# Kernel tuning notes

Measured on AMD Instinct MI355X. Metric: run time of the kernel, lower is better.

The kernel has to match this reference:

```python
import jax, jax.numpy as jnp
import numpy as np

CONF_THRES = 0.5   # self.conf_thres
NMS_THRES = 0.5    # self.nms_thres
PRE_NMS = 2048     # candidates kept before pairwise IoU
MAX_DET = 300      # padded detections returned per image
MAX_WH = 4096.0    # class-offset trick so NMS is per-class
IMG_SIZE = 416.0   # self.img_size; boxes_scale (416,416)->(416,416) => scale 1


def xywh2xyxy(b):
    xy, wh = b[..., :2], b[..., 2:4]
    return jnp.concatenate([xy - wh * 0.5, xy + wh * 0.5], axis=-1)


def pairwise_iou(boxes):
    # boxes: [K,4] xyxy -> [K,K] IoU
    area = (boxes[:, 2] - boxes[:, 0]) * (boxes[:, 3] - boxes[:, 1])
    lt = jnp.maximum(boxes[:, None, :2], boxes[None, :, :2])
    rb = jnp.minimum(boxes[:, None, 2:], boxes[None, :, 2:])
    wh = jnp.clip(rb - lt, 0.0)
    inter = wh[..., 0] * wh[..., 1]
    return inter / (area[:, None] + area[None, :] - inter + 1e-16)


def nms_single(pred):
    # pred: [N,85] = xywh(4) + objectness(1) + class scores(80)
    boxes = xywh2xyxy(pred[:, :4])
    obj = pred[:, 4]
    cls_scores = pred[:, 5:] * obj[:, None]        # conf = obj * class prob
    conf = jnp.max(cls_scores, axis=-1)
    cls_id = jnp.argmax(cls_scores, axis=-1)
    valid = obj >= CONF_THRES                      # confidence threshold filter
    score = jnp.where(valid, conf, -1.0)

    order = jnp.argsort(-score)[:PRE_NMS]          # sort desc, keep top PRE_NMS
    boxes_s = boxes[order]
    score_s = score[order]
    cls_s = cls_id[order]
    valid_s = valid[order]

    # per-class NMS via coordinate offset by class id
    off = cls_s.astype(boxes_s.dtype) * MAX_WH
    iou = pairwise_iou(boxes_s + off[:, None])     # [PRE_NMS, PRE_NMS]

    def body(keep, i):
        suppressed = jnp.any(keep & (iou[:, i] > NMS_THRES))
        k = valid_s[i] & ~suppressed
        return keep.at[i].set(k), k

    keep, _ = jax.lax.scan(body, jnp.zeros(PRE_NMS, dtype=bool), jnp.arange(PRE_NMS))

    final_score = jnp.where(keep, score_s, -1.0)
    top = jnp.argsort(-final_score)[:MAX_DET]
    kb, ks, kc, km = boxes_s[top], score_s[top], cls_s[top], keep[top]

    scale = IMG_SIZE / 416.0                       # boxes_scale (identity here)
    det = jnp.concatenate(
        [kb * scale, ks[:, None], kc[:, None].astype(kb.dtype)], axis=-1)
    return jnp.where(km[:, None], det, 0.0)        # [MAX_DET, 6] padded


def setup_inputs() -> dict:
    key = jax.random.key(0)
    predictions = jax.random.uniform(key, (16, 10647, 85), dtype=jnp.float32)
    return {"predictions": predictions}


def reference(predictions):
    # detections per image: [x1,y1,x2,y2,score,class], zero-padded to MAX_DET
    return jax.vmap(nms_single)(predictions)  # [B, MAX_DET, 6]
```

## Files before the change

### kernel.cpp

```cpp
#include <hip/hip_runtime.h>
#include <hip/hip_bf16.h>
#include <stdint.h>

typedef unsigned long long u64;
typedef unsigned int u32;
typedef unsigned short u16;

#define NANCH 10647
#define NBATCH 16
#define NSORT 16384
#define NSEL 2048
#define NWORD 32
#define NCLS 80
#define CONF_T 0.5f
#define NMS_T 0.5f
#define MAXDET 300
#define MAXWH 4096.0f

__global__ __launch_bounds__(256) void k_prep(const float* __restrict__ pred,
                                              u64* __restrict__ keys,
                                              float4* __restrict__ boxes,
                                              int* __restrict__ cls,
                                              float* __restrict__ score) {
    __shared__ float sm[128 * 85];
    int b = blockIdx.y;
    int a0 = blockIdx.x * 128;
    int na = NANCH - a0; if (na > 128) na = 128;
    const float* src = pred + ((size_t)b * NANCH + a0) * 85;
    int tot = na * 85;
    for (int i = threadIdx.x; i < tot; i += 256) sm[i] = src[i];
    __syncthreads();
    int t = threadIdx.x;
    if (t < na) {
        const float* s = &sm[t * 85];
        float x = s[0], y = s[1], w = s[2], h = s[3], obj = s[4];
        float best = s[5] * obj; int arg = 0;
        #pragma unroll
        for (int c = 1; c < 80; ++c) {
            float v = s[5 + c] * obj;
            if (v > best) { best = v; arg = c; }
        }
        bool valid = obj >= CONF_T;
        float sc = valid ? best : -1.0f;
        int a = a0 + t;
        float4 bx;
        bx.x = x - w * 0.5f; bx.y = y - h * 0.5f;
        bx.z = x + w * 0.5f; bx.w = y + h * 0.5f;
        size_t o = (size_t)b * NANCH + a;
        boxes[o] = bx;
        cls[o] = arg;
        score[o] = sc;
        u32 u = __float_as_uint(sc);
        u32 v = (u & 0x80000000u) ? ~u : (u | 0x80000000u);
        u32 hi = ~v;
        keys[(size_t)b * NSORT + a] = ((u64)hi << 32) | (u32)a;
    }
}

__global__ __launch_bounds__(1024) void k_sel(const u64* __restrict__ keys,
                                              const float4* __restrict__ boxes,
                                              const int* __restrict__ cls,
                                              const float* __restrict__ score,
                                              float4* __restrict__ sel_box,
                                              float4* __restrict__ sel_sbox,
                                              float* __restrict__ sel_area,
                                              float* __restrict__ sel_score,
                                              int* __restrict__ sel_cls) {
    __shared__ u64 sk[NSEL];
    __shared__ u32 hist[256];
    __shared__ u32 hsc[256];
    __shared__ u64 s_P;
    __shared__ u64 s_M;
    __shared__ u32 s_rank;
    __shared__ u32 s_cnt;

    int b = blockIdx.x;
    int tid = threadIdx.x;
    const u64* KB = keys + (size_t)b * NSORT;

    if (tid == 0) { s_P = 0; s_M = 0; s_rank = NSEL; s_cnt = 0; }
    __syncthreads();

    const int shifts[6] = {56, 48, 40, 32, 8, 0};
    for (int r = 0; r < 6; ++r) {
        int shift = shifts[r];
        if (tid < 256) hist[tid] = 0;
        __syncthreads();
        u64 P = s_P, M = s_M;
        for (int i = tid; i < NANCH; i += 1024) {
            u64 key = KB[i];
            if ((key & M) == P)
                atomicAdd(&hist[(u32)(key >> shift) & 0xFFu], 1u);
        }
        __syncthreads();
        if (tid < 256) hsc[tid] = hist[tid];
        __syncthreads();
        for (int d = 1; d < 256; d <<= 1) {
            u32 add = 0;
            if (tid < 256 && tid >= d) add = hsc[tid - d];
            __syncthreads();
            if (tid < 256) hsc[tid] += add;
            __syncthreads();
        }
        if (tid < 256) {
            u32 rank = s_rank;
            u32 inc = hsc[tid];
            u32 cb = inc - hist[tid];
            if (cb < rank && rank <= inc) {
                s_rank = rank - cb;
                s_P = s_P | ((u64)tid << shift);
                s_M = s_M | (0xFFull << shift);
            }
        }
        __syncthreads();
    }
    u64 T = s_P;

    for (int i = tid; i < NANCH; i += 1024) {
        u64 key = KB[i];
        if (key <= T) {
            u32 pos = atomicAdd(&s_cnt, 1u);
            sk[pos] = key;
        }
    }
    __syncthreads();

    for (int k = 2; k <= NSEL; k <<= 1) {
        for (int j = k >> 1; j > 0; j >>= 1) {
            int n = tid;
            int i = ((n & ~(j - 1)) << 1) | (n & (j - 1));
            int l = i | j;
            u64 a = sk[i], c = sk[l];
            bool up = ((i & k) == 0);
            if ((a > c) == up) { sk[i] = c; sk[l] = a; }
            __syncthreads();
        }
    }

    for (int r = tid; r < NSEL; r += 1024) {
        u64 key = sk[r];
        int a = (int)(key & 0xFFFFFFFFu);
        size_t src = (size_t)b * NANCH + a;
        float4 bx = boxes[src];
        int c = cls[src];
        float sc = score[src];
        float off = (float)c * MAXWH;
        float4 sb;
        sb.x = bx.x + off; sb.y = bx.y + off;
        sb.z = bx.z + off; sb.w = bx.w + off;
        float area = (sb.z - sb.x) * (sb.w - sb.y);
        size_t o = (size_t)b * NSEL + r;
        sel_box[o] = bx; sel_sbox[o] = sb; sel_area[o] = area;
        sel_score[o] = sc; sel_cls[o] = c;
    }
}

__global__ __launch_bounds__(1024) void k_cnms(const float4* __restrict__ sel_sbox,
                                               const float* __restrict__ sel_area,
                                               const int* __restrict__ sel_cls,
                                               const float* __restrict__ sel_score,
                                               u64* __restrict__ gkeep) {
    __shared__ u16 wmem[16][NSEL];
    __shared__ u64 wkeep[16][NWORD];

    int b = blockIdx.y;
    int cg = blockIdx.x;
    int lane = threadIdx.x & 63, wv = threadIdx.x >> 6;
    int c = cg * 16 + wv;
    size_t bb = (size_t)b * NSEL;
    const int* CL = sel_cls + bb;
    const float* SC = sel_score + bb;
    u64 below = (1ULL << lane) - 1ULL;

    int n = 0;
    for (int ch = 0; ch < NWORD; ++ch) {
        int i = ch * 64 + lane;
        bool pred = (CL[i] == c) && (SC[i] >= 0.0f);
        u64 bal = __ballot(pred);
        if (pred) wmem[wv][n + __popcll(bal & below)] = (u16)i;
        n += __popcll(bal);
    }

    for (int c0 = 0; c0 < n; c0 += 64) {
        int chunkn = n - c0; if (chunkn > 64) chunkn = 64;
        bool mv = lane < chunkn;
        int q = mv ? (int)wmem[wv][c0 + lane] : 0;
        float4 bq = sel_sbox[bb + q];
        float aq = sel_area[bb + q];

        bool hit = false;
        for (int j = 0; j < c0; ++j) {
            if (!((wkeep[wv][j >> 6] >> (j & 63)) & 1ULL)) continue;
            int p = (int)wmem[wv][j];
            float4 bp = sel_sbox[bb + p];
            float ap = sel_area[bb + p];
            float ltx = fmaxf(bp.x, bq.x), lty = fmaxf(bp.y, bq.y);
            float rbx = fminf(bp.z, bq.z), rby = fminf(bp.w, bq.w);
            float ww = fmaxf(rbx - ltx, 0.0f), hh = fmaxf(rby - lty, 0.0f);
            float inter = ww * hh;
            hit = hit || (mv && (inter / (ap + aq - inter + 1e-16f) > NMS_T));
        }
        u64 avail = __ballot(mv && !hit);

        u64 Rt = 0;
        for (int t = 0; t < chunkn; ++t) {
            int p = (int)wmem[wv][c0 + t];
            float4 bp = sel_sbox[bb + p];
            float ap = sel_area[bb + p];
            float ltx = fmaxf(bp.x, bq.x), lty = fmaxf(bp.y, bq.y);
            float rbx = fminf(bp.z, bq.z), rby = fminf(bp.w, bq.w);
            float ww = fmaxf(rbx - ltx, 0.0f), hh = fmaxf(rby - lty, 0.0f);
            float inter = ww * hh;
            u64 row = __ballot(mv && (inter / (ap + aq - inter + 1e-16f) > NMS_T));
            if (lane == t) Rt = row;
        }

        u64 U = avail, kept = 0;
        while (U) {
            bool inU = ((U >> lane) & 1ULL) != 0ULL;
            u64 newk = __ballot(inU && ((Rt & U & below) == 0ULL));
            u64 killed = __ballot((Rt & newk) != 0ULL);
            kept |= newk;
            U &= ~(newk | killed);
        }
        if (lane == 0) wkeep[wv][c0 >> 6] = kept;
        if ((kept >> lane) & 1ULL)
            atomicOr(&gkeep[(size_t)b * NWORD + (q >> 6)], 1ULL << (q & 63));
    }
}

__global__ __launch_bounds__(64) void k_out(const u64* __restrict__ gkeep,
                                            const float4* __restrict__ sel_box,
                                            const float* __restrict__ sel_score,
                                            const int* __restrict__ sel_cls,
                                            float* __restrict__ out) {
    int b = blockIdx.x;
    int lane = threadIdx.x;
    const float* SC = sel_score + (size_t)b * NSEL;
    u64 kreg = (lane < NWORD) ? gkeep[(size_t)b * NWORD + lane] : 0ULL;

    int cnt = (lane < NWORD) ? __popcll(kreg) : 0;
    int pre = cnt;
    #pragma unroll
    for (int dd = 1; dd < 64; dd <<= 1) {
        int o = __shfl_up(pre, dd);
        if (lane >= dd) pre += o;
    }
    int total = __shfl(pre, 63);
    int base = pre - cnt;
    float* OUT = out + (size_t)b * MAXDET * 6;
    if (lane < NWORD) {
        u64 m = kreg;
        int rr = 0;
        while (m) {
            int t = __ffsll((long long)m) - 1;
            m &= m - 1;
            int slot = base + rr; ++rr;
            if (slot < MAXDET) {
                int i = lane * 64 + t;
                size_t src = (size_t)b * NSEL + i;
                float4 bx = sel_box[src];
                float sc = SC[i];
                int c = sel_cls[src];
                float* o6 = OUT + slot * 6;
                o6[0] = bx.x; o6[1] = bx.y; o6[2] = bx.z; o6[3] = bx.w;
                o6[4] = sc; o6[5] = (float)c;
            }
        }
    }
    int start = total > MAXDET ? MAXDET : total;
    for (int s = start + lane; s < MAXDET; s += 64) {
        float* o6 = OUT + s * 6;
        o6[0] = 0.0f; o6[1] = 0.0f; o6[2] = 0.0f;
        o6[3] = 0.0f; o6[4] = 0.0f; o6[5] = 0.0f;
    }
}

extern "C" void kernel_launch(void* const* d_in, const int* in_sizes, int n_in,
                              void* d_out, int out_size, void* d_ws, size_t ws_size,
                              hipStream_t stream) {
    const float* pred = (const float*)d_in[0];
    float* out = (float*)d_out;

    char* ws = (char*)d_ws;
    size_t off = 0;
    auto alloc = [&](size_t bytes) -> void* {
        void* p = ws + off;
        off += (bytes + 255) & ~(size_t)255;
        return p;
    };

    u64*    keys      = (u64*)   alloc((size_t)NBATCH * NSORT * 8);
    float4* boxes     = (float4*)alloc((size_t)NBATCH * NANCH * 16);
    int*    cls       = (int*)   alloc((size_t)NBATCH * NANCH * 4);
    float*  score     = (float*) alloc((size_t)NBATCH * NANCH * 4);
    float4* sel_box   = (float4*)alloc((size_t)NBATCH * NSEL * 16);
    float4* sel_sbox  = (float4*)alloc((size_t)NBATCH * NSEL * 16);
    float*  sel_area  = (float*) alloc((size_t)NBATCH * NSEL * 4);
    float*  sel_score = (float*) alloc((size_t)NBATCH * NSEL * 4);
    int*    sel_cls   = (int*)   alloc((size_t)NBATCH * NSEL * 4);
    u64*    gkeep     = (u64*)   alloc((size_t)NBATCH * NWORD * 8);

    dim3 g1((NANCH + 127) / 128, NBATCH);
    k_prep<<<g1, 256, 0, stream>>>(pred, keys, boxes, cls, score);

    k_sel<<<NBATCH, 1024, 0, stream>>>(keys, boxes, cls, score,
                                       sel_box, sel_sbox, sel_area,
                                       sel_score, sel_cls);

    hipMemsetAsync(gkeep, 0, (size_t)NBATCH * NWORD * 8, stream);

    dim3 g3(5, NBATCH);
    k_cnms<<<g3, 1024, 0, stream>>>(sel_sbox, sel_area, sel_cls, sel_score, gkeep);

    k_out<<<NBATCH, 64, 0, stream>>>(gkeep, sel_box, sel_score, sel_cls, out);
}
```

Measured before the change: 112.3 us.

## Fuse top-byte histogram into prep and compact candidates for radix select

The prep kernel now builds the top-byte histogram of the sort keys with wave-aggregated shared atomics and adds it to a global per-image histogram. The select kernel uses that histogram to pick the pivot digit, then compacts keys into definite winners and a shared-memory candidate buffer. Later radix passes scan only the candidates rather than all 10647 keys again, and scans use shuffle-based prefix sums. This removes repeated full-array passes and many serial syncs, at the cost of more shared memory, extra global atomics and a larger memset.

```diff
diff --git a/kernel.cpp b/kernel.cpp
--- a/kernel.cpp
+++ b/kernel.cpp
@@ -16,21 +16,26 @@
 #define NMS_T 0.5f
 #define MAXDET 300
 #define MAXWH 4096.0f
+#define CANDCAP 10688
 
 __global__ __launch_bounds__(256) void k_prep(const float* __restrict__ pred,
                                               u64* __restrict__ keys,
                                               float4* __restrict__ boxes,
                                               int* __restrict__ cls,
-                                              float* __restrict__ score) {
+                                              float* __restrict__ score,
+                                              u32* __restrict__ ghist) {
     __shared__ float sm[128 * 85];
+    __shared__ u32 ph[256];
     int b = blockIdx.y;
     int a0 = blockIdx.x * 128;
     int na = NANCH - a0; if (na > 128) na = 128;
     const float* src = pred + ((size_t)b * NANCH + a0) * 85;
     int tot = na * 85;
+    ph[threadIdx.x] = 0;
     for (int i = threadIdx.x; i < tot; i += 256) sm[i] = src[i];
     __syncthreads();
     int t = threadIdx.x;
+    u64 kk = 0;
     if (t < na) {
         const float* s = &sm[t * 85];
         float x = s[0], y = s[1], w = s[2], h = s[3], obj = s[4];
@@ -53,11 +58,25 @@
         u32 u = __float_as_uint(sc);
         u32 v = (u & 0x80000000u) ? ~u : (u | 0x80000000u);
         u32 hi = ~v;
-        keys[(size_t)b * NSORT + a] = ((u64)hi << 32) | (u32)a;
-    }
+        kk = ((u64)hi << 32) | (u32)a;
+        keys[(size_t)b * NSORT + a] = kk;
+    }
+    u32 bin = (t < na) ? (u32)(kk >> 56) : 0xFFFFFFFFu;
+    int lane = t & 63;
+    u64 rem = __ballot(t < na);
+    while (rem) {
+        int srcl = __ffsll((long long)rem) - 1;
+        u32 lb = __shfl(bin, srcl);
+        u64 same = __ballot(bin == lb) & rem;
+        if (lane == srcl) atomicAdd(&ph[lb], (u32)__popcll(same));
+        rem &= ~same;
+    }
+    __syncthreads();
+    if (ph[threadIdx.x]) atomicAdd(&ghist[(size_t)b * 256 + threadIdx.x], ph[threadIdx.x]);
 }
 
 __global__ __launch_bounds__(1024) void k_sel(const u64* __restrict__ keys,
+                                              const u32* __restrict__ ghist,
                                               const float4* __restrict__ boxes,
                                               const int* __restrict__ cls,
                                               const float* __restrict__ score,
@@ -67,61 +86,132 @@
                                               float* __restrict__ sel_score,
                                               int* __restrict__ sel_cls) {
     __shared__ u64 sk[NSEL];
+    __shared__ u64 cand[CANDCAP];
     __shared__ u32 hist[256];
     __shared__ u32 hsc[256];
-    __shared__ u64 s_P;
-    __shared__ u64 s_M;
-    __shared__ u32 s_rank;
-    __shared__ u32 s_cnt;
+    __shared__ u64 s_red[16];
+    __shared__ u32 s_D0, s_D, s_rank, s_cnt, s_cand;
 
     int b = blockIdx.x;
     int tid = threadIdx.x;
+    int lane = tid & 63;
+    u64 below = (1ULL << lane) - 1ULL;
     const u64* KB = keys + (size_t)b * NSORT;
 
-    if (tid == 0) { s_P = 0; s_M = 0; s_rank = NSEL; s_cnt = 0; }
-    __syncthreads();
-
-    const int shifts[6] = {56, 48, 40, 32, 8, 0};
-    for (int r = 0; r < 6; ++r) {
-        int shift = shifts[r];
+    if (tid == 0) { s_cnt = 0; s_cand = 0; }
+    for (int i = tid; i < NSEL; i += 1024) sk[i] = ~0ULL;
+    if (tid < 256) hist[tid] = ghist[(size_t)b * 256 + tid];
+    __syncthreads();
+    if (tid < 64) {
+        u32 h0 = hist[tid*4], h1 = hist[tid*4+1], h2 = hist[tid*4+2], h3 = hist[tid*4+3];
+        u32 loc = h0 + h1 + h2 + h3;
+        u32 p = loc;
+        #pragma unroll
+        for (int o = 1; o < 64; o <<= 1) { u32 t2 = __shfl_up(p, o); if (lane >= o) p += t2; }
+        u32 base = p - loc;
+        hsc[tid*4]   = base + h0;
+        hsc[tid*4+1] = base + h0 + h1;
+        hsc[tid*4+2] = base + h0 + h1 + h2;
+        hsc[tid*4+3] = base + h0 + h1 + h2 + h3;
+    }
+    __syncthreads();
+    if (tid < 256) {
+        u32 inc = hsc[tid], cb = inc - hist[tid];
+        if (cb < NSEL && NSEL <= inc) { s_D0 = tid; s_rank = NSEL - cb; }
+    }
+    __syncthreads();
+    u32 D0 = s_D0;
+
+    for (int it = 0; it < 11; ++it) {
+        int i = tid + it * 1024;
+        bool inb = i < NANCH;
+        u64 kk = inb ? KB[i] : 0ULL;
+        u32 top = (u32)(kk >> 56);
+        bool is_s = inb && (top < D0);
+        bool is_c = inb && (top == D0);
+        u64 bs = __ballot(is_s), bc = __ballot(is_c);
+        u32 base_s = 0, base_c = 0;
+        if (lane == 0) {
+            if (bs) base_s = atomicAdd(&s_cnt, (u32)__popcll(bs));
+            if (bc) base_c = atomicAdd(&s_cand, (u32)__popcll(bc));
+        }
+        base_s = __shfl(base_s, 0); base_c = __shfl(base_c, 0);
+        if (is_s) sk[base_s + __popcll(bs & below)] = kk;
+        if (is_c) cand[base_c + __popcll(bc & below)] = kk;
+    }
+    __syncthreads();
+
+    const int shifts2[5] = {48, 40, 32, 8, 0};
+    for (int rr = 0; ; ++rr) {
+        u32 cn = s_cand, r = s_rank;
+        if (r == cn || rr == 5) {
+            for (u32 i0 = 0; i0 < cn; i0 += 1024) {
+                u32 i = i0 + tid;
+                bool take = i < cn;
+                u64 kk = take ? cand[i] : 0ULL;
+                u64 bt = __ballot(take);
+                u32 base = 0;
+                if (lane == 0 && bt) base = atomicAdd(&s_cnt, (u32)__popcll(bt));
+                base = __shfl(base, 0);
+                if (take) sk[base + __popcll(bt & below)] = kk;
+            }
+            break;
+        }
+        if (r == 1) {
+            u64 best = ~0ULL;
+            for (u32 i = tid; i < cn; i += 1024) { u64 kk = cand[i]; if (kk < best) best = kk; }
+            #pragma unroll
+            for (int o = 32; o > 0; o >>= 1) {
+                u64 other = __shfl_down(best, o);
+                if (other < best) best = other;
+            }
+            if (lane == 0) s_red[tid >> 6] = best;
+            __syncthreads();
+            if (tid == 0) {
+                u64 m = s_red[0];
+                for (int w2 = 1; w2 < 16; ++w2) if (s_red[w2] < m) m = s_red[w2];
+                sk[atomicAdd(&s_cnt, 1u)] = m;
+            }
+            break;
+        }
+        int shift = shifts2[rr];
         if (tid < 256) hist[tid] = 0;
         __syncthreads();
-        u64 P = s_P, M = s_M;
-        for (int i = tid; i < NANCH; i += 1024) {
-            u64 key = KB[i];
-            if ((key & M) == P)
-                atomicAdd(&hist[(u32)(key >> shift) & 0xFFu], 1u);
-        }
-        __syncthreads();
-        if (tid < 256) hsc[tid] = hist[tid];
-        __syncthreads();
-        for (int d = 1; d < 256; d <<= 1) {
-            u32 add = 0;
-            if (tid < 256 && tid >= d) add = hsc[tid - d];
-            __syncthreads();
-            if (tid < 256) hsc[tid] += add;
-            __syncthreads();
-        }
+        for (u32 i = tid; i < cn; i += 1024)
+            atomicAdd(&hist[(u32)(cand[i] >> shift) & 0xFFu], 1u);
+        __syncthreads();
+        if (tid < 64) {
+            u32 h0 = hist[tid*4], h1 = hist[tid*4+1], h2 = hist[tid*4+2], h3 = hist[tid*4+3];
+            u32 loc = h0 + h1 + h2 + h3;
+            u32 p = loc;
+            #pragma unroll
+            for (int o = 1; o < 64; o <<= 1) { u32 t2 = __shfl_up(p, o); if (lane >= o) p += t2; }
+            u32 base = p - loc;
+            hsc[tid*4]   = base + h0;
+            hsc[tid*4+1] = base + h0 + h1;
+            hsc[tid*4+2] = base + h0 + h1 + h2;
+            hsc[tid*4+3] = base + h0 + h1 + h2 + h3;
+        }
+        __syncthreads();
         if (tid < 256) {
-            u32 rank = s_rank;
-            u32 inc = hsc[tid];
-            u32 cb = inc - hist[tid];
-            if (cb < rank && rank <= inc) {
-                s_rank = rank - cb;
-                s_P = s_P | ((u64)tid << shift);
-                s_M = s_M | (0xFFull << shift);
-            }
-        }
-        __syncthreads();
-    }
-    u64 T = s_P;
-
-    for (int i = tid; i < NANCH; i += 1024) {
-        u64 key = KB[i];
-        if (key <= T) {
-            u32 pos = atomicAdd(&s_cnt, 1u);
-            sk[pos] = key;
-        }
+            u32 inc = hsc[tid], cb = inc - hist[tid];
+            if (cb < r && r <= inc) { s_D = tid; s_rank = r - cb; }
+        }
+        __syncthreads();
+        u32 D = s_D;
+        u64 mk[11], mc[11]; int nk = 0, nc = 0;
+        for (u32 i = tid; i < cn; i += 1024) {
+            u64 kk = cand[i];
+            u32 dg = (u32)(kk >> shift) & 0xFFu;
+            if (dg < D) mk[nk++] = kk;
+            else if (dg == D) mc[nc++] = kk;
+        }
+        __syncthreads();
+        if (tid == 0) s_cand = 0;
+        __syncthreads();
+        if (nk) { u32 p = atomicAdd(&s_cnt, (u32)nk); for (int j = 0; j < nk; ++j) sk[p + j] = mk[j]; }
+        if (nc) { u32 p = atomicAdd(&s_cand, (u32)nc); for (int j = 0; j < nc; ++j) cand[p + j] = mc[j]; }
+        __syncthreads();
     }
     __syncthreads();
 
@@ -137,9 +227,10 @@
         }
     }
 
-    for (int r = tid; r < NSEL; r += 1024) {
-        u64 key = sk[r];
+    for (int r2 = tid; r2 < NSEL; r2 += 1024) {
+        u64 key = sk[r2];
         int a = (int)(key & 0xFFFFFFFFu);
+        if ((unsigned)a >= NANCH) a = 0;
         size_t src = (size_t)b * NANCH + a;
         float4 bx = boxes[src];
         int c = cls[src];
@@ -149,7 +240,7 @@
         sb.x = bx.x + off; sb.y = bx.y + off;
         sb.z = bx.z + off; sb.w = bx.w + off;
         float area = (sb.z - sb.x) * (sb.w - sb.y);
-        size_t o = (size_t)b * NSEL + r;
+        size_t o = (size_t)b * NSEL + r2;
         sel_box[o] = bx; sel_sbox[o] = sb; sel_area[o] = area;
         sel_score[o] = sc; sel_cls[o] = c;
     }
@@ -300,16 +391,17 @@
     float*  sel_score = (float*) alloc((size_t)NBATCH * NSEL * 4);
     int*    sel_cls   = (int*)   alloc((size_t)NBATCH * NSEL * 4);
     u64*    gkeep     = (u64*)   alloc((size_t)NBATCH * NWORD * 8);
+    u32*    ghist     = (u32*)   alloc((size_t)NBATCH * 256 * 4);
+
+    hipMemsetAsync(gkeep, 0, (size_t)NBATCH * NWORD * 8 + (size_t)NBATCH * 256 * 4, stream);
 
     dim3 g1((NANCH + 127) / 128, NBATCH);
-    k_prep<<<g1, 256, 0, stream>>>(pred, keys, boxes, cls, score);
-
-    k_sel<<<NBATCH, 1024, 0, stream>>>(keys, boxes, cls, score,
+    k_prep<<<g1, 256, 0, stream>>>(pred, keys, boxes, cls, score, ghist);
+
+    k_sel<<<NBATCH, 1024, 0, stream>>>(keys, ghist, boxes, cls, score,
                                        sel_box, sel_sbox, sel_area,
                                        sel_score, sel_cls);
 
-    hipMemsetAsync(gkeep, 0, (size_t)NBATCH * NWORD * 8, stream);
-
     dim3 g3(5, NBATCH);
     k_cnms<<<g3, 1024, 0, stream>>>(sel_sbox, sel_area, sel_cls, sel_score, gkeep);
 
```

Measured after the change: 109.0 us. -2.9%, faster.
